# Optimization experiments

Hardware: AMD Instinct MI355X
Metric: run time of the kernel (lower is better)

The kernel has to match this reference:

```python
import jax, jax.numpy as jnp
import numpy as np

B, ARITY = 4096, 6
EMB = 100
NF = 200
FC = 1200
N_ROLES, N_VALUES = 5000, 50000
BN_EPS = 1e-5


def setup_inputs() -> dict:
    key = jax.random.key(0)
    ks = jax.random.split(key, 12)
    bound = float(np.sqrt(1.0 / EMB))
    x = jax.random.randint(ks[0], (B, 2 * ARITY), 0, 5000, dtype=jnp.int64)
    emb_roles = jax.random.uniform(ks[1], (N_ROLES, EMB), jnp.float32, -bound, bound)
    emb_values = jax.random.uniform(ks[2], (N_VALUES, EMB), jnp.float32, -bound, bound)
    conv_w = 0.1 * jax.random.normal(ks[3], (NF, 2 * EMB), jnp.float32)  # conv (1,2E) kernel == linear
    conv_b = jnp.zeros((NF,), jnp.float32)
    bn_gamma = jnp.ones((NF,), jnp.float32)
    bn_beta = jnp.zeros((NF,), jnp.float32)
    gW = jax.random.normal(ks[4], (FC, 2 * NF), jnp.float32) * float(np.sqrt(2.0 / (FC + 2 * NF)))
    gb = jnp.zeros((FC,), jnp.float32)
    fW = jax.random.normal(ks[5], (1, FC), jnp.float32) * float(np.sqrt(2.0 / (1 + FC)))
    fb = jnp.zeros((1,), jnp.float32)
    return dict(x=x, emb_roles=emb_roles, emb_values=emb_values, conv_w=conv_w,
                conv_b=conv_b, bn_gamma=bn_gamma, bn_beta=bn_beta,
                gW=gW, gb=gb, fW=fW, fb=fb)


def reference(x, emb_roles, emb_values, conv_w, conv_b, bn_gamma, bn_beta, gW, gb, fW, fb):
    arity = x.shape[1] // 2
    roles = emb_roles[x[:, 0::2]]    # [B, A, E]
    values = emb_values[x[:, 1::2]]  # [B, A, E]
    cat = jnp.concatenate([roles, values], axis=-1)  # [B, A, 2E]
    # conv1 with kernel (1, 2E) == per-row linear 2E -> NF
    m = jnp.einsum('bae,fe->baf', cat, conv_w) + conv_b  # [B, A, NF]
    # BatchNorm2d (training mode: batch statistics over B and A per channel)
    mu = m.mean(axis=(0, 1))
    var = m.var(axis=(0, 1))
    m = (m - mu) * jax.lax.rsqrt(var + BN_EPS) * bn_gamma + bn_beta
    m_rel = jax.nn.relu(m)  # [B, A, NF]
    # all role-value pairs: first tiles the sequence, second repeats each row
    first = jnp.tile(m_rel, (1, arity, 1))           # [B, A*A, NF]
    second = jnp.repeat(m_rel, arity, axis=1)        # [B, A*A, NF]
    pairs = jnp.concatenate([first, second], axis=-1)  # [B, A*A, 2NF]
    g = jax.nn.relu(jnp.einsum('bpf,of->bpo', pairs, gW) + gb)  # [B, A*A, FC]
    min_val = g.min(axis=1)  # [B, FC]
    score = min_val @ fW.T + fb  # [B, 1]
    return score
```

## Files before the change

kernel.cpp:

```cpp
#include <hip/hip_runtime.h>
#include <hip/hip_bf16.h>
#include <hip/hip_fp16.h>

#define B_    4096
#define ARITY 6
#define EMB   100
#define NF    200
#define FC    1200
#define NROWS (B_*ARITY)
#define MPAD  (B_*8)
#define NPAD  2432
#define BN_EPS 1e-5f
#define KP    224
#define SENT  32768.0f
#define NTW   (NPAD/4/16)

typedef _Float16 half8 __attribute__((ext_vector_type(8)));
typedef float f32x4 __attribute__((ext_vector_type(4)));

#define MRAW_OFF 0
#define WH_OFF   2457600
#define WT_OFF   2729984
#define STAT_OFF 2780160

__device__ __forceinline__ float4 ld4(const float* rr, const float* vr, int e) {
    if (e < EMB)        return *(const float4*)&rr[e];
    else if (e < 2*EMB) return *(const float4*)&vr[e - EMB];
    float4 z = {0.f,0.f,0.f,0.f}; return z;
}

#define K0_W1 (224*28)
#define K0_W2 (K0_W1 + NPAD*28)
#define K0_TOT (K0_W2 + B_)
__launch_bounds__(256)
__global__ void k0_prep(const float* __restrict__ cw, const float* __restrict__ gW,
                        const float* __restrict__ fb,
                        _Float16* __restrict__ wT,
                        _Float16* __restrict__ W_h, float* __restrict__ out)
{
    int id = blockIdx.x * 256 + threadIdx.x;
    if (id < K0_W1) {
        int f = id / 28, s = id - f*28;
        int ks = s >> 2, ls = s & 3;
        int off = ks*14336 + (f >> 4)*512 + (f & 15)*32 + ls*8;
        half8 h, l;
        #pragma unroll
        for (int j = 0; j < 8; ++j) {
            int k = s*8 + j;
            float v = (f < NF && k < NF) ? cw[f*NF + k] : 0.f;
            _Float16 hi = (_Float16)v;
            h[j] = hi; l[j] = (_Float16)(v - (float)hi);
        }
        *(half8*)&wT[off] = h;
        *(half8*)&wT[off + 7168] = l;
    } else if (id < K0_W2) {
        int id2 = id - K0_W1;
        int n = id2 / 28, s = id2 - n*28;
        int o = n >> 1, hf = n & 1;
        int off = (n >> 4)*3584 + (s >> 2)*512 + (n & 15)*32 + (s & 3)*8;
        half8 h;
        #pragma unroll
        for (int j = 0; j < 8; ++j) {
            int k = s*8 + j;
            float v = 0.f;
            if (k < NF && n < 2*FC) v = gW[(size_t)o*400 + hf*200 + k];
            if (k == NF) v = SENT;
            h[j] = (_Float16)v;
        }
        *(half8*)&W_h[off] = h;
    } else if (id < K0_TOT) {
        out[id - K0_W2] = fb[0];
    }
}

__launch_bounds__(256, 3)
__global__ void k1_mfma(const int* __restrict__ x,
                        const float* __restrict__ er,
                        const float* __restrict__ ev,
                        const _Float16* __restrict__ wT,
                        const float* __restrict__ cb,
                        _Float16* __restrict__ m_raw,
                        float* __restrict__ gshad)
{
    __shared__ __align__(16) char smem[30528];
    _Float16* s_ahi = (_Float16*)smem;
    _Float16* s_alo = s_ahi + 7168;
    float* s_sum = (float*)(smem + 28672);
    float* s_sq  = (float*)(smem + 29472);
    int*   s_ri  = (int*)(smem + 30272);
    int*   s_vi  = (int*)(smem + 30400);

    const int t = threadIdx.x, lane = t & 63, wave = t >> 6;
    const int wm = wave >> 1, wn = wave & 1;
    const int R0 = blockIdx.x * 32;
    const int q = lane >> 4, cx = lane & 15;
    const int rdsw = (q ^ ((cx >> 1) & 3)) * 8;

    if (t < 32) {
        int R = R0 + t, b = R / ARITY, a = R - b * ARITY;
        bool is64 = ((x[1] | x[3] | x[5] | x[7]) == 0);
        int base = b * (2*ARITY) + 2*a;
        s_ri[t] = is64 ? x[2*base]     : x[base];
        s_vi[t] = is64 ? x[2*base + 2] : x[base + 1];
    }
    if (t < NF) { s_sum[t] = 0.f; s_sq[t] = 0.f; }
    __syncthreads();

    for (int c = t; c < 896; c += 256) {
        int row = c / 28, s = c - row*28;
        int key = (row >> 1) & 3;
        int col = (s >> 2)*32 + ((s & 3) ^ key)*8;
        const float* rr = er + (size_t)s_ri[row] * EMB;
        const float* vr = ev + (size_t)s_vi[row] * EMB;
        int e0 = s*8;
        float4 v0 = ld4(rr, vr, e0);
        float4 v1 = ld4(rr, vr, e0 + 4);
        half8 hi, lo;
        hi[0]=(_Float16)v0.x; lo[0]=(_Float16)(v0.x-(float)hi[0]);
        hi[1]=(_Float16)v0.y; lo[1]=(_Float16)(v0.y-(float)hi[1]);
        hi[2]=(_Float16)v0.z; lo[2]=(_Float16)(v0.z-(float)hi[2]);
        hi[3]=(_Float16)v0.w; lo[3]=(_Float16)(v0.w-(float)hi[3]);
        hi[4]=(_Float16)v1.x; lo[4]=(_Float16)(v1.x-(float)hi[4]);
        hi[5]=(_Float16)v1.y; lo[5]=(_Float16)(v1.y-(float)hi[5]);
        hi[6]=(_Float16)v1.z; lo[6]=(_Float16)(v1.z-(float)hi[6]);
        hi[7]=(_Float16)v1.w; lo[7]=(_Float16)(v1.w-(float)hi[7]);
        *(half8*)&s_ahi[row*KP + col] = hi;
        *(half8*)&s_alo[row*KP + col] = lo;
    }
    __syncthreads();

    f32x4 ah[7], al[7];
    {
        int arow = wm*16 + cx;
        #pragma unroll
        for (int ks = 0; ks < 7; ++ks) {
            ah[ks] = *(const f32x4*)&s_ahi[arow*KP + ks*32 + rdsw];
            al[ks] = *(const f32x4*)&s_alo[arow*KP + ks*32 + rdsw];
        }
    }

    f32x4 acc[7];
    #pragma unroll
    for (int nf = 0; nf < 7; ++nf) acc[nf] = (f32x4){0.f,0.f,0.f,0.f};

    #pragma unroll
    for (int ks = 0; ks < 7; ++ks) {
        #pragma unroll
        for (int nf = 0; nf < 7; ++nf) {
            const _Float16* wp = wT + ks*14336 + (wn*7 + nf)*512 + cx*32 + q*8;
            f32x4 bh = *(const f32x4*)wp;
            f32x4 bl = *(const f32x4*)(wp + 7168);
            acc[nf] = __builtin_amdgcn_mfma_f32_16x16x32_f16(
                __builtin_bit_cast(half8, ah[ks]),
                __builtin_bit_cast(half8, bh), acc[nf], 0,0,0);
            acc[nf] = __builtin_amdgcn_mfma_f32_16x16x32_f16(
                __builtin_bit_cast(half8, ah[ks]),
                __builtin_bit_cast(half8, bl), acc[nf], 0,0,0);
            acc[nf] = __builtin_amdgcn_mfma_f32_16x16x32_f16(
                __builtin_bit_cast(half8, al[ks]),
                __builtin_bit_cast(half8, bh), acc[nf], 0,0,0);
        }
    }

    #pragma unroll
    for (int nf = 0; nf < 7; ++nf) {
        int f = wn*112 + nf*16 + cx;
        bool valid = (f < NF);
        float bias = valid ? cb[f] : 0.f;
        float ps = 0.f, pq = 0.f;
        #pragma unroll
        for (int reg = 0; reg < 4; ++reg) {
            float vv = acc[nf][reg] + bias;
            if (valid) {
                int R = R0 + wm*16 + q*4 + reg;
                m_raw[(size_t)R*NF + f] = (_Float16)vv;
                ps += vv; pq += vv*vv;
            }
        }
        ps += __shfl_xor(ps, 16); ps += __shfl_xor(ps, 32);
        pq += __shfl_xor(pq, 16); pq += __shfl_xor(pq, 32);
        if (valid && q == 0) { atomicAdd(&s_sum[f], ps); atomicAdd(&s_sq[f], pq); }
    }
    __syncthreads();
    if (t < NF) {
        float* g = gshad + (blockIdx.x & 15) * 400;
        atomicAdd(&g[t], s_sum[t]);
        atomicAdd(&g[t + 200], s_sq[t]);
    }
}

__launch_bounds__(256, 2)
__global__ void k3_mfma(const _Float16* __restrict__ m_raw,
                        const float* __restrict__ gshad,
                        const float* __restrict__ gamma,
                        const float* __restrict__ beta,
                        const _Float16* __restrict__ W_h,
                        const float* __restrict__ gb,
                        const float* __restrict__ fW,
                        float* __restrict__ out)
{
    __shared__ __align__(16) char smem[40192];
    float2* gbfw2 = (float2*)(smem + 28672);
    float*  scsh  = (float*)(smem + 28672 + 9728);

    const int t = threadIdx.x, lane = t & 63, wave = t >> 6;
    const int q = lane >> 4, cx = lane & 15;
    const int rdsw = (q ^ ((cx >> 1) & 3)) * 8;

    if (t < 224) {
        float sc = 0.f, sh = 0.f;
        if (t < NF) {
            float s = 0.f, qq = 0.f;
            #pragma unroll
            for (int c = 0; c < 16; ++c) { s += gshad[c*400 + t]; qq += gshad[c*400 + 200 + t]; }
            float inv = 1.0f / (float)NROWS;
            float mu  = s * inv;
            float var = qq * inv - mu*mu;
            float rs  = rsqrtf(var + BN_EPS);
            sc = rs * gamma[t];
            sh = beta[t] - mu*sc;
        }
        scsh[t] = sc; scsh[224 + t] = sh;
    }
    for (int i = t; i < 1216; i += 256) {
        float g = (i < FC) ? gb[i] : 0.f;
        float f = (i < FC) ? fW[i] : 0.f;
        gbfw2[i] = make_float2(g, f);
    }
    __syncthreads();

    {
        _Float16* sa = (_Float16*)smem;
        for (int c = t; c < 1792; c += 256) {
            int Rp = c / 28, s = c - Rp*28;
            int a = Rp & 7, b = Rp >> 3;
            int key = (Rp >> 1) & 3;
            int col = (s >> 2)*32 + ((s & 3) ^ key)*8;
            half8 o;
            #pragma unroll
            for (int j = 0; j < 8; ++j) o[j] = (_Float16)0.f;
            if (a < ARITY && s < 25) {
                int R = (blockIdx.x*8 + b)*ARITY + a;
                half8 in = *(const half8*)&m_raw[(size_t)R*NF + s*8];
                #pragma unroll
                for (int j = 0; j < 8; ++j) {
                    int k = s*8 + j;
                    o[j] = (_Float16)fmaxf((float)in[j]*scsh[k] + scsh[224+k], 0.f);
                }
            } else if (a >= ARITY && s == 25) {
                o[0] = (_Float16)1.0f;
            }
            *(half8*)&sa[Rp*KP + col] = o;
        }
    }
    __syncthreads();

    f32x4 av[4][7];
    {
        const _Float16* sa = (const _Float16*)smem;
        #pragma unroll
        for (int mf = 0; mf < 4; ++mf) {
            int row = mf*16 + cx;
            #pragma unroll
            for (int ks = 0; ks < 7; ++ks)
                av[mf][ks] = *(const f32x4*)&sa[row*KP + ks*32 + rdsw];
        }
    }

    const int nbase = wave * (NPAD/4);
    const char* wsrc = (const char*)W_h + (size_t)nbase * 448;
    const int boff = cx*64 + q*16;

    #define LOADT(BV_, NT_) do {                                             \
        const char* _b = wsrc + (size_t)(NT_)*7168 + boff;                   \
        _Pragma("unroll")                                                    \
        for (int _k = 0; _k < 7; ++_k)                                       \
            BV_[_k] = *(const f32x4*)(_b + _k*1024);                         \
    } while (0)

    #define MFMAT(BV_, ACC_) do {                                            \
        _Pragma("unroll")                                                    \
        for (int _m = 0; _m < 4; ++_m) ACC_[_m] = (f32x4){0.f,0.f,0.f,0.f};  \
        _Pragma("unroll")                                                    \
        for (int _k = 0; _k < 7; ++_k) {                                     \
            _Pragma("unroll")                                                \
            for (int _m = 0; _m < 4; ++_m)                                   \
                ACC_[_m] = __builtin_amdgcn_mfma_f32_16x16x32_f16(           \
                    __builtin_bit_cast(half8, av[_m][_k]),                   \
                    __builtin_bit_cast(half8, BV_[_k]), ACC_[_m], 0, 0, 0);  \
        }                                                                    \
    } while (0)

    float preg[4] = {0.f, 0.f, 0.f, 0.f};

    #define EPI(ACC_, NT_) do {                                              \
        float2 _gf = gbfw2[(nbase + (NT_)*16 + cx) >> 1];                    \
        _Pragma("unroll")                                                    \
        for (int _m = 0; _m < 4; ++_m) {                                     \
            f32x4 _a4 = ACC_[_m];                                            \
            float _v = fminf(fminf(_a4[0], _a4[1]), fminf(_a4[2], _a4[3]));  \
            _v = fminf(_v, __shfl_xor(_v, 16));         \
            float _vp = _v + __shfl_xor(_v, 1);            \
            float _val = fmaxf(_vp + _gf.x, 0.f) * _gf.y;                    \
            if (((q & 1) == 0) && ((cx & 1) == 0)) preg[_m] += _val;         \
        }                                                                    \
    } while (0)

    f32x4 bv0[7], bv1[7];
    f32x4 acc0[4], acc1[4];

    LOADT(bv0, 0);
    LOADT(bv1, 1);
    MFMAT(bv0, acc0);
    for (int k = 0; k < 17; ++k) {
        int nt = 2*k + 1;
        LOADT(bv0, nt + 1); MFMAT(bv1, acc1); EPI(acc0, nt - 1);
        LOADT(bv1, nt + 2); MFMAT(bv0, acc0); EPI(acc1, nt);
    }
    LOADT(bv0, 36); MFMAT(bv1, acc1); EPI(acc0, 34);
    LOADT(bv1, 37); MFMAT(bv0, acc0); EPI(acc1, 35);
    MFMAT(bv1, acc1); EPI(acc0, 36);
    EPI(acc1, 37);

    #pragma unroll
    for (int mf = 0; mf < 4; ++mf) {
        float v = preg[mf];
        v += __shfl_xor(v, 2);
        v += __shfl_xor(v, 4);
        v += __shfl_xor(v, 8);
        if (cx == 0 && (q & 1) == 0) {
            int bb = blockIdx.x*8 + mf*2 + (q >> 1);
            atomicAdd(&out[bb], v);
        }
    }
}

extern "C" void kernel_launch(void* const* d_in, const int* in_sizes, int n_in,
                              void* d_out, int out_size, void* d_ws, size_t ws_size,
                              hipStream_t stream)
{
    const int*   x   = (const int*)  d_in[0];
    const float* er  = (const float*)d_in[1];
    const float* ev  = (const float*)d_in[2];
    const float* cw  = (const float*)d_in[3];
    const float* cb  = (const float*)d_in[4];
    const float* gam = (const float*)d_in[5];
    const float* bet = (const float*)d_in[6];
    const float* gW  = (const float*)d_in[7];
    const float* gb  = (const float*)d_in[8];
    const float* fW  = (const float*)d_in[9];
    const float* fb  = (const float*)d_in[10];

    float* ws = (float*)d_ws;
    _Float16* m_raw = (_Float16*)(ws + MRAW_OFF);
    _Float16* W_h   = (_Float16*)(ws + WH_OFF);
    _Float16* wT    = (_Float16*)(ws + WT_OFF);
    float* gshad    = ws + STAT_OFF;
    float* out      = (float*)d_out;

    (void)hipMemsetAsync(gshad, 0, 16*400*sizeof(float), stream);

    k0_prep<<<(K0_TOT + 255)/256, 256, 0, stream>>>(cw, gW, fb, wT, W_h, out);
    k1_mfma<<<NROWS/32, 256, 0, stream>>>(x, er, ev, wT, cb, m_raw, gshad);
    k3_mfma<<<MPAD/64, 256, 0, stream>>>(m_raw, gshad, gam, bet, W_h, gb, fW, out);
}
```

Before: 82.66 us.

## Double-buffer weight loads and interleave epilogue per N-fragment in k1

Restructures the k1 GEMM loop from ks-outer/nf-inner into nf-outer with all 7 K-steps per fragment. Weight fragments for the next N-tile are loaded into a second register buffer while the current one feeds MFMAs, and each fragment's epilogue (bias, fp16 store, BN partial sums) runs right after its accumulation. This aims to hide global weight-load latency and overlap epilogue stores with MFMA work. The larger register footprint forces launch bounds down from 3 to 2 blocks per SM, which reduces occupancy.

```diff
diff --git a/kernel.cpp b/kernel.cpp
--- a/kernel.cpp
+++ b/kernel.cpp
@@ -73,7 +73,7 @@
     }
 }
 
-__launch_bounds__(256, 3)
+__launch_bounds__(256, 2)
 __global__ void k1_mfma(const int* __restrict__ x,
                         const float* __restrict__ er,
                         const float* __restrict__ ev,
@@ -139,48 +139,68 @@
         }
     }
 
-    f32x4 acc[7];
-    #pragma unroll
-    for (int nf = 0; nf < 7; ++nf) acc[nf] = (f32x4){0.f,0.f,0.f,0.f};
-
-    #pragma unroll
-    for (int ks = 0; ks < 7; ++ks) {
-        #pragma unroll
-        for (int nf = 0; nf < 7; ++nf) {
-            const _Float16* wp = wT + ks*14336 + (wn*7 + nf)*512 + cx*32 + q*8;
-            f32x4 bh = *(const f32x4*)wp;
-            f32x4 bl = *(const f32x4*)(wp + 7168);
-            acc[nf] = __builtin_amdgcn_mfma_f32_16x16x32_f16(
-                __builtin_bit_cast(half8, ah[ks]),
-                __builtin_bit_cast(half8, bh), acc[nf], 0,0,0);
-            acc[nf] = __builtin_amdgcn_mfma_f32_16x16x32_f16(
-                __builtin_bit_cast(half8, ah[ks]),
-                __builtin_bit_cast(half8, bl), acc[nf], 0,0,0);
-            acc[nf] = __builtin_amdgcn_mfma_f32_16x16x32_f16(
-                __builtin_bit_cast(half8, al[ks]),
-                __builtin_bit_cast(half8, bh), acc[nf], 0,0,0);
-        }
-    }
-
-    #pragma unroll
-    for (int nf = 0; nf < 7; ++nf) {
-        int f = wn*112 + nf*16 + cx;
-        bool valid = (f < NF);
-        float bias = valid ? cb[f] : 0.f;
-        float ps = 0.f, pq = 0.f;
-        #pragma unroll
-        for (int reg = 0; reg < 4; ++reg) {
-            float vv = acc[nf][reg] + bias;
-            if (valid) {
-                int R = R0 + wm*16 + q*4 + reg;
-                m_raw[(size_t)R*NF + f] = (_Float16)vv;
-                ps += vv; pq += vv*vv;
-            }
-        }
-        ps += __shfl_xor(ps, 16); ps += __shfl_xor(ps, 32);
-        pq += __shfl_xor(pq, 16); pq += __shfl_xor(pq, 32);
-        if (valid && q == 0) { atomicAdd(&s_sum[f], ps); atomicAdd(&s_sq[f], pq); }
-    }
+    const _Float16* wbase = wT + (wn*7)*512 + cx*32 + q*8;
+
+    #define LOADW(BH_, BL_, NF_) do {                                        \
+        _Pragma("unroll")                                                    \
+        for (int _k = 0; _k < 7; ++_k) {                                     \
+            const _Float16* _p = wbase + _k*14336 + (NF_)*512;               \
+            BH_[_k] = *(const f32x4*)_p;                                     \
+            BL_[_k] = *(const f32x4*)(_p + 7168);                            \
+        }                                                                    \
+    } while (0)
+
+    #define MFMAW(BH_, BL_, ACC_) do {                                       \
+        ACC_ = (f32x4){0.f,0.f,0.f,0.f};                                     \
+        _Pragma("unroll")                                                    \
+        for (int _k = 0; _k < 7; ++_k) {                                     \
+            ACC_ = __builtin_amdgcn_mfma_f32_16x16x32_f16(                   \
+                __builtin_bit_cast(half8, ah[_k]),                           \
+                __builtin_bit_cast(half8, BH_[_k]), ACC_, 0,0,0);            \
+            ACC_ = __builtin_amdgcn_mfma_f32_16x16x32_f16(                   \
+                __builtin_bit_cast(half8, ah[_k]),                           \
+                __builtin_bit_cast(half8, BL_[_k]), ACC_, 0,0,0);            \
+            ACC_ = __builtin_amdgcn_mfma_f32_16x16x32_f16(                   \
+                __builtin_bit_cast(half8, al[_k]),                           \
+                __builtin_bit_cast(half8, BH_[_k]), ACC_, 0,0,0);            \
+        }                                                                    \
+    } while (0)
+
+    #define EPIW(ACC_, NF_) do {                                             \
+        int _f = wn*112 + (NF_)*16 + cx;                                     \
+        bool _valid = (_f < NF);                                             \
+        float _bias = _valid ? cb[_f] : 0.f;                                 \
+        float _ps = 0.f, _pq = 0.f;                                          \
+        _Pragma("unroll")                                                    \
+        for (int _r = 0; _r < 4; ++_r) {                                     \
+            float _vv = ACC_[_r] + _bias;                                    \
+            if (_valid) {                                                    \
+                int _R = R0 + wm*16 + q*4 + _r;                              \
+                m_raw[(size_t)_R*NF + _f] = (_Float16)_vv;                   \
+                _ps += _vv; _pq += _vv*_vv;                                  \
+            }                                                                \
+        }                                                                    \
+        _ps += __shfl_xor(_ps, 16); _ps += __shfl_xor(_ps, 32);              \
+        _pq += __shfl_xor(_pq, 16); _pq += __shfl_xor(_pq, 32);              \
+        if (_valid && q == 0) {                                              \
+            atomicAdd(&s_sum[_f], _ps); atomicAdd(&s_sq[_f], _pq);           \
+        }                                                                    \
+    } while (0)
+
+    f32x4 bh0[7], bl0[7], bh1[7], bl1[7];
+    f32x4 accA, accB;
+
+    LOADW(bh0, bl0, 0);
+    LOADW(bh1, bl1, 1);
+    MFMAW(bh0, bl0, accA);
+    LOADW(bh0, bl0, 2); MFMAW(bh1, bl1, accB); EPIW(accA, 0);
+    LOADW(bh1, bl1, 3); MFMAW(bh0, bl0, accA); EPIW(accB, 1);
+    LOADW(bh0, bl0, 4); MFMAW(bh1, bl1, accB); EPIW(accA, 2);
+    LOADW(bh1, bl1, 5); MFMAW(bh0, bl0, accA); EPIW(accB, 3);
+    LOADW(bh0, bl0, 6); MFMAW(bh1, bl1, accB); EPIW(accA, 4);
+    MFMAW(bh0, bl0, accA); EPIW(accB, 5);
+    EPIW(accA, 6);
+
     __syncthreads();
     if (t < NF) {
         float* g = gshad + (blockIdx.x & 15) * 400;
```

New measurement: 86.96 us. 5.2% more time.
